# Kernel optimization log

Hardware: AMD Instinct MI355X
Metric: run time of the kernel (lower is better)

Reference implementation:

```python
import jax, jax.numpy as jnp
import numpy as np

N, E, D, H, G, L, EF = 50000, 800000, 128, 256, 512, 3, 8
BN_EPS = 1e-5


def _bn(h, g, b):
    # torch BatchNorm1d in training mode: biased batch stats over the node axis
    m = h.mean(0)
    v = h.var(0)
    return g * (h - m) * jax.lax.rsqrt(v + BN_EPS) + b


def setup_inputs() -> dict:
    ks = jax.random.split(jax.random.key(0), 12)
    sc = 0.05
    return {
        "x": jax.random.normal(ks[0], (N, D), jnp.float32),
        "edge_attr": jax.random.normal(ks[1], (E, EF), jnp.float32),
        "vn_emb": jnp.zeros((1, D), jnp.float32),  # init.constant_(0)
        "We": jax.random.normal(ks[2], (L, EF, D)) * sc,
        "be": jnp.zeros((L, D)),
        "W1": jax.random.normal(ks[3], (L, D, H)) * sc,
        "b1": jnp.zeros((L, H)),
        "g1": jnp.ones((L, H)),
        "bt1": jnp.zeros((L, H)),
        "W2": jax.random.normal(ks[4], (L, H, D)) * sc,
        "b2": jnp.zeros((L, D)),
        "gb": jnp.ones((L, D)),
        "bb": jnp.zeros((L, D)),
        "Wv1": jax.random.normal(ks[5], (L - 1, D, H)) * sc,
        "bv1": jnp.zeros((L - 1, H)),
        "gv1": jnp.ones((L - 1, H)),
        "btv1": jnp.zeros((L - 1, H)),
        "Wv2": jax.random.normal(ks[6], (L - 1, H, D)) * sc,
        "bv2": jnp.zeros((L - 1, D)),
        "gv2": jnp.ones((L - 1, D)),
        "btv2": jnp.zeros((L - 1, D)),
        "edge_index": jax.random.randint(ks[7], (2, E), 0, N),
        "batch": jnp.sort(jax.random.randint(ks[8], (N,), 0, G)),
    }


def reference(x, edge_attr, vn_emb, We, be, W1, b1, g1, bt1, W2, b2, gb, bb,
              Wv1, bv1, gv1, btv1, Wv2, bv2, gv2, btv2, edge_index, batch):
    src, dst = edge_index[0], edge_index[1]
    vn = jnp.broadcast_to(vn_emb, (G, D))  # Embedding(1, D) looked up for every graph
    h = x  # node_encoder is None -> encoded_node = x
    for l in range(L):
        h_in = h + vn[batch]                              # virtual-node broadcast (gather)
        e = edge_attr @ We[l] + be[l]                     # per-layer edge encoder
        msg = jax.nn.relu(h_in[src] + e)                  # GIN message, [E, D]
        aggr = jax.ops.segment_sum(msg, dst, num_segments=N)
        z = h_in + aggr                                   # (1+eps)*h + aggr, eps=0
        z = jax.nn.relu(_bn(z @ W1[l] + b1[l], g1[l], bt1[l]))
        h = _bn(z @ W2[l] + b2[l], gb[l], bb[l])          # conv MLP out + outer BatchNorm
        if l < L - 1:
            h = jax.nn.relu(h)                            # dropout ratio 0 -> identity
            pooled = jax.ops.segment_sum(h_in, batch, num_segments=G) + vn
            t = jax.nn.relu(_bn(pooled @ Wv1[l] + bv1[l], gv1[l], btv1[l]))
            vn = jax.nn.relu(_bn(t @ Wv2[l] + bv2[l], gv2[l], btv2[l]))
    return h  # JK == 'last'
```

## Files before the change

### kernel.cpp

```cpp
#include <hip/hip_runtime.h>
#include <hip/hip_bf16.h>

#define N_NODES 50000
#define N_EDGES 800000
#define DIM 128
#define HID 256
#define N_GRAPH 512
#define N_LAYER 3
#define EFEAT 8
#define BN_EPS 1e-5f
#define MAX_GROUPS 240000
#define AGGR_WAVES 8192

typedef unsigned short u16;
typedef unsigned int u32;

using bf16x8_t = short __attribute__((ext_vector_type(8)));
using f32x4_t  = float __attribute__((ext_vector_type(4)));
using f32x2    = float __attribute__((ext_vector_type(2)));
using f32x4v   = float __attribute__((ext_vector_type(4)));


__device__ __forceinline__ void atomic_add_f(float* p, float v) {
    unsafeAtomicAdd(p, v);
}
__device__ __forceinline__ u16 f2bf(float x) {
    union { float f; u32 u; } v; v.f = x;
    u32 r = v.u + 0x7FFF + ((v.u >> 16) & 1);
    return (u16)(r >> 16);
}
__device__ __forceinline__ float bf2f(u16 u) {
    union { u32 i; float f; } v; v.i = (u32)u << 16; return v.f;
}
__device__ __forceinline__ float2 up2(u32 p) {
    return make_float2(bf2f((u16)(p & 0xFFFF)), bf2f((u16)(p >> 16)));
}
__device__ __forceinline__ u32 pk2(float a, float b) {
    return (u32)f2bf(a) | ((u32)f2bf(b) << 16);
}
__device__ __forceinline__ f32x2 up2p(u32 p) {
    union { u32 u[2]; f32x2 f; } v;
    v.u[0] = p << 16;
    v.u[1] = p & 0xFFFF0000u;
    return v.f;
}
__device__ __forceinline__ f32x2 splat2(float x) {
    f32x2 r; r.x = x; r.y = x; return r;
}

__global__ __launch_bounds__(256) void wconv_kernel(
    const float* __restrict__ W1, const float* __restrict__ W2,
    u16* __restrict__ W1t, u16* __restrict__ W2t)
{
    int idx = blockIdx.x * 256 + threadIdx.x;
    if (idx >= 6 * 32768) return;
    int m = idx >> 15;
    int off = idx & 32767;
    int l = m >> 1;
    if ((m & 1) == 0) {
        int r = off >> 8, c = off & 255;
        W1t[(size_t)l * 32768 + c * 128 + r] = f2bf(W1[(size_t)l * 32768 + r * 256 + c]);
    } else {
        int r = off >> 7, c = off & 127;
        W2t[(size_t)l * 32768 + c * 256 + r] = f2bf(W2[(size_t)l * 32768 + r * 128 + c]);
    }
}

__global__ __launch_bounds__(256) void hist_rank_kernel(
    const int* __restrict__ ei, int* __restrict__ deg, int* __restrict__ rank)
{
    int e = blockIdx.x * 256 + threadIdx.x;
    if (e >= N_EDGES) return;
    int dst = ei[N_EDGES + e];
    rank[e] = atomicAdd(&deg[dst], 1);
}

__global__ __launch_bounds__(1024) void scan_kernel(const int* __restrict__ deg, int* __restrict__ grpptr) {
    __shared__ int wsum[16];
    __shared__ int carry;
    int tid = threadIdx.x;
    if (tid == 0) { carry = 0; grpptr[0] = 0; }
    __syncthreads();
    for (int base = 0; base < N_NODES; base += 1024) {
        int i = base + tid;
        int v = (i < N_NODES) ? ((deg[i] + 3) >> 2) : 0;
        int lane = tid & 63, w = tid >> 6;
        int s = v;
        #pragma unroll
        for (int d = 1; d < 64; d <<= 1) { int t = __shfl_up(s, d); if (lane >= d) s += t; }
        if (lane == 63) wsum[w] = s;
        __syncthreads();
        if (tid < 64) {
            int t = (tid < 16) ? wsum[tid] : 0;
            #pragma unroll
            for (int d = 1; d < 16; d <<= 1) { int u = __shfl_up(t, d); if (tid >= d) t += u; }
            if (tid < 16) wsum[tid] = t;
        }
        __syncthreads();
        int excl = (w > 0) ? wsum[w - 1] : 0;
        int incl = s + excl + carry;
        if (i < N_NODES) grpptr[i + 1] = incl;
        __syncthreads();
        if (tid == 0) carry += wsum[15];
        __syncthreads();
    }
}

__global__ __launch_bounds__(256) void padinit_kernel(uint4* __restrict__ rec4, int nq) {
    int i = blockIdx.x * 256 + threadIdx.x;
    if (i >= nq) return;
    u32 s = (u32)N_NODES << 8;
    rec4[i] = make_uint4(s, 0u, s, 0u);
}

__global__ void negrow_kernel(u16* __restrict__ hin) {
    int l = threadIdx.x;
    *(u32*)(hin + (size_t)N_NODES * DIM + l * 2) = 0xFF7FFF7Fu;
}

__global__ __launch_bounds__(256) void scatter_kernel(
    const int* __restrict__ ei,
    const int* __restrict__ rank, const int* __restrict__ grpptr,
    uint2* __restrict__ srec)
{
    int e = blockIdx.x * 256 + threadIdx.x;
    if (e >= N_EDGES) return;
    int src = __builtin_nontemporal_load(ei + e);
    int dst = __builtin_nontemporal_load(ei + N_EDGES + e);
    int rk  = __builtin_nontemporal_load(rank + e);
    int slot = grpptr[dst] * 4 + rk;
    slot = (grpptr[dst] + (rk >> 2)) * 4 + (rk & 3);
    uint2 v;
    v.x = (u32)src << 8;
    v.y = (u32)e << 5;
    srec[slot] = v;
}

__global__ __launch_bounds__(256) void expand_kernel(
    const uint2* __restrict__ srec, const float* __restrict__ ea,
    char* __restrict__ brec, int nslots)
{
    int i = blockIdx.x * 256 + threadIdx.x;
    if (i >= nslots) return;
    int g = i >> 2;
    int j = i & 3;
    uint2 v = srec[i];
    const char* eaB = (const char*)ea;
    f32x4v lo = *(const f32x4v*)(eaB + v.y);
    f32x4v hi = *(const f32x4v*)(eaB + v.y + 16);
    char* rb = brec + (size_t)g * 144;
    *(u32*)(rb + j * 4) = v.x;
    *(f32x4v*)(rb + 16 + j * 32) = lo;
    *(f32x4v*)(rb + 32 + j * 32) = hi;
}

__global__ __launch_bounds__(256) void wstart_kernel(
    const int* __restrict__ grpptr, int* __restrict__ wstart)
{
    int w = blockIdx.x * 256 + threadIdx.x;
    if (w > AGGR_WAVES) return;
    if (w == AGGR_WAVES) { wstart[w] = N_NODES; return; }
    int Gt = grpptr[N_NODES];
    int q = (int)(((long long)w * Gt) / AGGR_WAVES);
    int lo = 0, hi = N_NODES;
    while (lo < hi) { int mid = (lo + hi) >> 1; if (grpptr[mid] < q) lo = mid + 1; else hi = mid; }
    wstart[w] = lo;
}

template <bool USEBN, int VNM>
__global__ __launch_bounds__(256) void hin_kernel(
    const float* __restrict__ src,
    const float* __restrict__ sum2, const float* __restrict__ ss2,
    const float* __restrict__ g, const float* __restrict__ b, float invN,
    const int* __restrict__ batch,
    const float* __restrict__ vn_emb,
    const float* __restrict__ vnpre, const float* __restrict__ vsum, const float* __restrict__ vss,
    const float* __restrict__ gv, const float* __restrict__ btv, float invG,
    u16* __restrict__ hin, int total4)
{
    int idx = blockIdx.x * 256 + threadIdx.x;
    if (idx >= total4) return;
    int base = idx * 4;
    int n = base >> 7;
    int c = base & (DIM - 1);
    float4 v = *(const float4*)(src + base);
    float o[4] = {v.x, v.y, v.z, v.w};
    if (USEBN) {
        #pragma unroll
        for (int j = 0; j < 4; ++j) {
            int cj = c + j;
            float m = sum2[cj] * invN;
            float var = ss2[cj] * invN - m * m;
            float r = rsqrtf(var + BN_EPS);
            float a = g[cj] * r;
            o[j] = fmaxf(fmaf(a, o[j], b[cj] - m * a), 0.f);
        }
    }
    int grp = batch[n];
    if (VNM == 0) {
        const float4 w = *(const float4*)(vn_emb + c);
        o[0] += w.x; o[1] += w.y; o[2] += w.z; o[3] += w.w;
    } else {
        const float4 vp = *(const float4*)(vnpre + (size_t)grp * DIM + c);
        float vv[4] = {vp.x, vp.y, vp.z, vp.w};
        #pragma unroll
        for (int j = 0; j < 4; ++j) {
            int cj = c + j;
            float m = vsum[cj] * invG;
            float var = vss[cj] * invG - m * m;
            float r = rsqrtf(var + BN_EPS);
            float a = gv[cj] * r;
            o[j] += fmaxf(fmaf(a, vv[j], btv[cj] - m * a), 0.f);
        }
    }
    uint2 pk;
    pk.x = pk2(o[0], o[1]);
    pk.y = pk2(o[2], o[3]);
    *(uint2*)(hin + base) = pk;
}

__device__ __forceinline__ void edge_term_f(
    u32 h, f32x4v ea, f32x4v eb, const f32x2* rW, f32x2 rB, f32x2& acc)
{
    f32x2 ex = rB;
    ex = __builtin_elementwise_fma(splat2(ea.x), rW[0], ex);
    ex = __builtin_elementwise_fma(splat2(ea.y), rW[1], ex);
    ex = __builtin_elementwise_fma(splat2(ea.z), rW[2], ex);
    ex = __builtin_elementwise_fma(splat2(ea.w), rW[3], ex);
    ex = __builtin_elementwise_fma(splat2(eb.x), rW[4], ex);
    ex = __builtin_elementwise_fma(splat2(eb.y), rW[5], ex);
    ex = __builtin_elementwise_fma(splat2(eb.z), rW[6], ex);
    ex = __builtin_elementwise_fma(splat2(eb.w), rW[7], ex);
    f32x2 s = up2p(h) + ex;
    s = __builtin_elementwise_max(s, splat2(0.f));
    acc += s;
}

__global__ __launch_bounds__(256) void aggr_kernel(
    const int* __restrict__ grpptr, const char* __restrict__ rec,
    const float* __restrict__ Wel, const float* __restrict__ bel,
    const u16* __restrict__ hin, u16* __restrict__ z,
    const int* __restrict__ wstart)
{
    const int lane = threadIdx.x & 63;
    const int cb = lane * 4;
    const int wid = __builtin_amdgcn_readfirstlane((blockIdx.x << 2) + (threadIdx.x >> 6));

    f32x2 rW[EFEAT];
    #pragma unroll
    for (int k = 0; k < EFEAT; ++k) {
        float2 t = *(const float2*)(Wel + k * DIM + lane * 2);
        rW[k].x = t.x; rW[k].y = t.y;
    }
    float2 tb = *(const float2*)(bel + lane * 2);
    f32x2 rB; rB.x = tb.x; rB.y = tb.y;

    const char* hinB = (const char*)hin;
    int n = wstart[wid];
    const int n1 = wstart[wid + 1];

    while (n < n1 && grpptr[n + 1] == grpptr[n]) {
        f32x2 a0 = up2p(*(const u32*)(hinB + ((u32)n << 8) + cb));
        *(u32*)(z + ((size_t)n << 7) + lane * 2) = pk2(a0.x, a0.y);
        ++n;
    }
    if (n < n1) {
        int g = grpptr[n];
        const int gTot = grpptr[n1];
        int gEnd = grpptr[n + 1];
        f32x2 acc = up2p(*(const u32*)(hinB + ((u32)n << 8) + cb));
        const char* rb = rec + (size_t)g * 144;

        uint4 so = *(const uint4*)rb;
        u32 h0 = *(const u32*)(hinB + so.x + cb);
        u32 h1 = *(const u32*)(hinB + so.y + cb);
        u32 h2 = *(const u32*)(hinB + so.z + cb);
        u32 h3 = *(const u32*)(hinB + so.w + cb);
        f32x4v e0a = *(const f32x4v*)(rb + 16);
        f32x4v e0b = *(const f32x4v*)(rb + 32);
        f32x4v e1a = *(const f32x4v*)(rb + 48);
        f32x4v e1b = *(const f32x4v*)(rb + 64);
        f32x4v e2a = *(const f32x4v*)(rb + 80);
        f32x4v e2b = *(const f32x4v*)(rb + 96);
        f32x4v e3a = *(const f32x4v*)(rb + 112);
        f32x4v e3b = *(const f32x4v*)(rb + 128);
        uint4 soN = *(const uint4*)(rb + 144);

        #pragma unroll 2
        for (; g < gTot; ++g, rb += 144) {
            u32 i0 = *(const u32*)(hinB + soN.x + cb);
            u32 i1 = *(const u32*)(hinB + soN.y + cb);
            u32 i2 = *(const u32*)(hinB + soN.z + cb);
            u32 i3 = *(const u32*)(hinB + soN.w + cb);
            f32x4v f0a = *(const f32x4v*)(rb + 160);
            f32x4v f0b = *(const f32x4v*)(rb + 176);
            f32x4v f1a = *(const f32x4v*)(rb + 192);
            f32x4v f1b = *(const f32x4v*)(rb + 208);
            f32x4v f2a = *(const f32x4v*)(rb + 224);
            f32x4v f2b = *(const f32x4v*)(rb + 240);
            f32x4v f3a = *(const f32x4v*)(rb + 256);
            f32x4v f3b = *(const f32x4v*)(rb + 272);
            uint4 soNN = *(const uint4*)(rb + 288);
            edge_term_f(h0, e0a, e0b, rW, rB, acc);
            edge_term_f(h1, e1a, e1b, rW, rB, acc);
            edge_term_f(h2, e2a, e2b, rW, rB, acc);
            edge_term_f(h3, e3a, e3b, rW, rB, acc);
            h0 = i0; h1 = i1; h2 = i2; h3 = i3;
            e0a = f0a; e0b = f0b; e1a = f1a; e1b = f1b;
            e2a = f2a; e2b = f2b; e3a = f3a; e3b = f3b;
            soN = soNN;
            if (g + 1 == gEnd) {
                *(u32*)(z + ((size_t)n << 7) + lane * 2) = pk2(acc.x, acc.y);
                ++n;
                if (g + 1 < gTot) {
                    while (grpptr[n + 1] == grpptr[n]) {
                        f32x2 a0 = up2p(*(const u32*)(hinB + ((u32)n << 8) + cb));
                        *(u32*)(z + ((size_t)n << 7) + lane * 2) = pk2(a0.x, a0.y);
                        ++n;
                    }
                    acc = up2p(*(const u32*)(hinB + ((u32)n << 8) + cb));
                    gEnd = grpptr[n + 1];
                }
            }
        }
    }
    while (n < n1) {
        f32x2 a0 = up2p(*(const u32*)(hinB + ((u32)n << 8) + cb));
        *(u32*)(z + ((size_t)n << 7) + lane * 2) = pk2(a0.x, a0.y);
        ++n;
    }
}

template <int MODE, bool CBF16>
__global__ __launch_bounds__(256) void gemm_bf16_kernel(
    const u16* __restrict__ Aa,
    const float* __restrict__ sSum, const float* __restrict__ sSS,
    const float* __restrict__ gA, const float* __restrict__ btA, float invCnt,
    const u16* __restrict__ Bt,
    const float* __restrict__ bias,
    void* __restrict__ CoutV,
    float* __restrict__ outSum, float* __restrict__ outSS,
    int M, int K, int Nc)
{
    constexpr int BM = 128, BN = 128, BK = 128;
    constexpr int LDA = BK + 8;
    __shared__ u16 As[BM * LDA];
    __shared__ u16 Bs[64 * LDA];
    __shared__ float csum[BN], css[BN];

    const int tid = threadIdx.x;
    const int wave = tid >> 6, lane = tid & 63;
    const int row0 = blockIdx.x * BM, col0 = blockIdx.y * BN;
    const int w_m = (wave & 1) * 64, w_n = (wave >> 1) * 32;
    const int quad = lane >> 4, l16 = lane & 15;

    if (tid < BN) { csum[tid] = 0.f; css[tid] = 0.f; }

    f32x4_t acc[4][4];
    #pragma unroll
    for (int mi = 0; mi < 4; ++mi)
        #pragma unroll
        for (int ni = 0; ni < 4; ++ni)
            acc[mi][ni] = (f32x4_t){0.f, 0.f, 0.f, 0.f};

    const int kc = (tid & 15) * 8;
    const int nkt = K / BK;

    for (int kt = 0; kt < nkt; ++kt) {
        float af[8], bf_[8];
        if (MODE == 1) {
            #pragma unroll
            for (int j = 0; j < 8; ++j) {
                int kg = kt * BK + kc + j;
                float m = sSum[kg] * invCnt;
                float var = sSS[kg] * invCnt - m * m;
                float r = rsqrtf(var + BN_EPS);
                float a = gA[kg] * r;
                af[j] = a;
                bf_[j] = btA[kg] - m * a;
            }
        }
        #pragma unroll
        for (int it = 0; it < 8; ++it) {
            int chunk = it * 256 + tid;
            int row = chunk >> 4;
            int gr = row0 + row; if (gr >= M) gr = M - 1;
            uint4 q = *(const uint4*)(Aa + (size_t)gr * K + kt * BK + kc);
            if (MODE == 1) {
                float2 p0 = up2(q.x), p1 = up2(q.y), p2 = up2(q.z), p3 = up2(q.w);
                p0.x = fmaxf(fmaf(af[0], p0.x, bf_[0]), 0.f);
                p0.y = fmaxf(fmaf(af[1], p0.y, bf_[1]), 0.f);
                p1.x = fmaxf(fmaf(af[2], p1.x, bf_[2]), 0.f);
                p1.y = fmaxf(fmaf(af[3], p1.y, bf_[3]), 0.f);
                p2.x = fmaxf(fmaf(af[4], p2.x, bf_[4]), 0.f);
                p2.y = fmaxf(fmaf(af[5], p2.y, bf_[5]), 0.f);
                p3.x = fmaxf(fmaf(af[6], p3.x, bf_[6]), 0.f);
                p3.y = fmaxf(fmaf(af[7], p3.y, bf_[7]), 0.f);
                q.x = pk2(p0.x, p0.y); q.y = pk2(p1.x, p1.y);
                q.z = pk2(p2.x, p2.y); q.w = pk2(p3.x, p3.y);
            }
            *(uint4*)(As + row * LDA + kc) = q;
        }
        #pragma unroll
        for (int half = 0; half < 2; ++half) {
            #pragma unroll
            for (int it = 0; it < 4; ++it) {
                int chunk = it * 256 + tid;
                int n = chunk >> 4;
                uint4 q = *(const uint4*)(Bt + (size_t)(col0 + half * 64 + n) * K + kt * BK + kc);
                *(uint4*)(Bs + n * LDA + kc) = q;
            }
            __syncthreads();
            #pragma unroll
            for (int ks = 0; ks < 4; ++ks) {
                bf16x8_t a_frag[4], b_frag[2];
                #pragma unroll
                for (int mi = 0; mi < 4; ++mi)
                    a_frag[mi] = *(const bf16x8_t*)(As + (w_m + mi * 16 + l16) * LDA + ks * 32 + quad * 8);
                #pragma unroll
                for (int ni = 0; ni < 2; ++ni)
                    b_frag[ni] = *(const bf16x8_t*)(Bs + (w_n + ni * 16 + l16) * LDA + ks * 32 + quad * 8);
                #pragma unroll
                for (int mi = 0; mi < 4; ++mi)
                    #pragma unroll
                    for (int ni = 0; ni < 2; ++ni)
                        acc[mi][half * 2 + ni] = __builtin_amdgcn_mfma_f32_16x16x32_bf16(
                            a_frag[mi], b_frag[ni], acc[mi][half * 2 + ni], 0, 0, 0);
            }
            __syncthreads();
        }
    }

    u16* Cb = (u16*)CoutV;
    float* Cf = (float*)CoutV;
    #pragma unroll
    for (int half = 0; half < 2; ++half)
    #pragma unroll
    for (int ni = 0; ni < 2; ++ni) {
        int ccol = half * 64 + w_n + ni * 16 + l16;
        int col = col0 + ccol;
        float bv = bias[col];
        float s = 0.f, qs = 0.f;
        #pragma unroll
        for (int mi = 0; mi < 4; ++mi) {
            int rbase = row0 + w_m + mi * 16 + quad * 4;
            #pragma unroll
            for (int reg = 0; reg < 4; ++reg) {
                int gr = rbase + reg;
                if (gr < M) {
                    float o = acc[mi][half * 2 + ni][reg] + bv;
                    s += o;
                    qs += o * o;
                    if (CBF16) Cb[(size_t)gr * Nc + col] = f2bf(o);
                    else       Cf[(size_t)gr * Nc + col] = o;
                }
            }
        }
        s += __shfl_xor(s, 16);  s += __shfl_xor(s, 32);
        qs += __shfl_xor(qs, 16);  qs += __shfl_xor(qs, 32);
        if (quad == 0) {
            atomicAdd(&csum[ccol], s);
            atomicAdd(&css[ccol], qs);
        }
    }
    __syncthreads();
    if (tid < BN) {
        atomic_add_f(outSum + col0 + tid, csum[tid]);
        atomic_add_f(outSS + col0 + tid, css[tid]);
    }
}

template <int MODE>
__global__ __launch_bounds__(256) void gemm_kernel(
    const float* __restrict__ Aa,
    const float* __restrict__ sSum, const float* __restrict__ sSS,
    const float* __restrict__ gA, const float* __restrict__ btA, float invCnt,
    const float* __restrict__ B, const float* __restrict__ bias,
    float* __restrict__ Cout, float* __restrict__ outSum, float* __restrict__ outSS,
    int M, int K, int Nc)
{
    __shared__ float As[16][68];
    __shared__ float Bs[16][64];
    __shared__ float alphaS[256], betaS[256];
    __shared__ float csum[64], css[64];

    const int tid = threadIdx.x;
    const int tx = tid & 15, ty = tid >> 4;
    const int row0 = blockIdx.x * 64, col0 = blockIdx.y * 64;

    if (tid < 64) { csum[tid] = 0.f; css[tid] = 0.f; }
    if (MODE == 1) {
        for (int k = tid; k < K; k += 256) {
            float m = sSum[k] * invCnt;
            float var = sSS[k] * invCnt - m * m;
            float r = rsqrtf(var + BN_EPS);
            float a = gA[k] * r;
            alphaS[k] = a;
            betaS[k] = btA[k] - m * a;
        }
    }
    __syncthreads();

    float acc[4][4];
    #pragma unroll
    for (int i = 0; i < 4; ++i)
        #pragma unroll
        for (int j = 0; j < 4; ++j) acc[i][j] = 0.f;

    const int lr = tid >> 2;
    const int lk = (tid & 3) * 4;
    const int bk = tid >> 4;
    const int bc = tx * 4;

    for (int kt = 0; kt < K; kt += 16) {
        int gr = row0 + lr;
        float4 va = make_float4(0.f, 0.f, 0.f, 0.f);
        if (gr < M) {
            va = *(const float4*)(Aa + (size_t)gr * K + kt + lk);
            if (MODE == 1) {
                int k0 = kt + lk;
                va.x = fmaxf(fmaf(alphaS[k0 + 0], va.x, betaS[k0 + 0]), 0.f);
                va.y = fmaxf(fmaf(alphaS[k0 + 1], va.y, betaS[k0 + 1]), 0.f);
                va.z = fmaxf(fmaf(alphaS[k0 + 2], va.z, betaS[k0 + 2]), 0.f);
                va.w = fmaxf(fmaf(alphaS[k0 + 3], va.w, betaS[k0 + 3]), 0.f);
            }
        }
        As[lk + 0][lr] = va.x;
        As[lk + 1][lr] = va.y;
        As[lk + 2][lr] = va.z;
        As[lk + 3][lr] = va.w;
        const float4 vb4 = *(const float4*)(B + (size_t)(kt + bk) * Nc + col0 + bc);
        *(float4*)&Bs[bk][bc] = vb4;
        __syncthreads();
        #pragma unroll
        for (int kk = 0; kk < 16; ++kk) {
            const float4 a4 = *(const float4*)&As[kk][ty * 4];
            const float4 b4 = *(const float4*)&Bs[kk][tx * 4];
            float av[4] = {a4.x, a4.y, a4.z, a4.w};
            float bv4[4] = {b4.x, b4.y, b4.z, b4.w};
            #pragma unroll
            for (int i = 0; i < 4; ++i)
                #pragma unroll
                for (int j = 0; j < 4; ++j)
                    acc[i][j] = fmaf(av[i], bv4[j], acc[i][j]);
        }
        __syncthreads();
    }

    const float4 bvv = *(const float4*)(bias + col0 + tx * 4);
    float bias4[4] = {bvv.x, bvv.y, bvv.z, bvv.w};
    float ps[4] = {0.f, 0.f, 0.f, 0.f};
    float pq[4] = {0.f, 0.f, 0.f, 0.f};
    #pragma unroll
    for (int i = 0; i < 4; ++i) {
        int gr = row0 + ty * 4 + i;
        if (gr < M) {
            float o[4];
            #pragma unroll
            for (int j = 0; j < 4; ++j) {
                o[j] = acc[i][j] + bias4[j];
                ps[j] += o[j];
                pq[j] += o[j] * o[j];
            }
            *(float4*)(Cout + (size_t)gr * Nc + col0 + tx * 4) = make_float4(o[0], o[1], o[2], o[3]);
        }
    }
    #pragma unroll
    for (int j = 0; j < 4; ++j) {
        atomicAdd(&csum[tx * 4 + j], ps[j]);
        atomicAdd(&css[tx * 4 + j], pq[j]);
    }
    __syncthreads();
    if (tid < 64) {
        atomic_add_f(outSum + col0 + tid, csum[tid]);
        atomic_add_f(outSS + col0 + tid, css[tid]);
    }
}

template <int VNM>
__global__ __launch_bounds__(64) void pooled_seg_kernel(
    const u16* __restrict__ hin, const int* __restrict__ batch,
    const float* __restrict__ vn_emb,
    const float* __restrict__ vnpre, const float* __restrict__ vsum, const float* __restrict__ vss,
    const float* __restrict__ gv, const float* __restrict__ btv, float invG,
    float* __restrict__ pooled)
{
    int g = blockIdx.x;
    int lane = threadIdx.x;
    int c2 = lane * 2;
    int lo = 0, hi = N_NODES;
    while (lo < hi) { int mid = (lo + hi) >> 1; if (batch[mid] < g) lo = mid + 1; else hi = mid; }
    int start = lo;
    hi = N_NODES;
    while (lo < hi) { int mid = (lo + hi) >> 1; if (batch[mid] < g + 1) lo = mid + 1; else hi = mid; }
    int end = lo;

    f32x2 acc;
    if (VNM == 0) {
        float2 w = *(const float2*)(vn_emb + c2);
        acc.x = w.x; acc.y = w.y;
    } else {
        float2 vs = *(const float2*)(vsum + c2);
        float2 vq = *(const float2*)(vss + c2);
        float2 gg = *(const float2*)(gv + c2);
        float2 bt = *(const float2*)(btv + c2);
        float2 vp = *(const float2*)(vnpre + (size_t)g * DIM + c2);
        float m0 = vs.x * invG, m1 = vs.y * invG;
        float va0 = vq.x * invG - m0 * m0, va1 = vq.y * invG - m1 * m1;
        float a0 = gg.x * rsqrtf(va0 + BN_EPS), a1 = gg.y * rsqrtf(va1 + BN_EPS);
        acc.x = fmaxf(fmaf(a0, vp.x, bt.x - m0 * a0), 0.f);
        acc.y = fmaxf(fmaf(a1, vp.y, bt.y - m1 * a1), 0.f);
    }

    const char* hinB = (const char*)hin;
    const int cb = lane * 4;
    f32x2 s0 = splat2(0.f), s1 = splat2(0.f), s2 = splat2(0.f), s3 = splat2(0.f);
    int n = start;
    for (; n + 3 < end; n += 4) {
        s0 += up2p(*(const u32*)(hinB + ((size_t)(n + 0) << 8) + cb));
        s1 += up2p(*(const u32*)(hinB + ((size_t)(n + 1) << 8) + cb));
        s2 += up2p(*(const u32*)(hinB + ((size_t)(n + 2) << 8) + cb));
        s3 += up2p(*(const u32*)(hinB + ((size_t)(n + 3) << 8) + cb));
    }
    for (; n < end; ++n) s0 += up2p(*(const u32*)(hinB + ((size_t)n << 8) + cb));
    acc += (s0 + s1) + (s2 + s3);
    *(float2*)(pooled + (size_t)g * DIM + c2) = make_float2(acc.x, acc.y);
}

__global__ __launch_bounds__(256) void final_bn_kernel(
    float* __restrict__ outp, const float* __restrict__ sum2, const float* __restrict__ ss2,
    const float* __restrict__ g, const float* __restrict__ b, float invN, int total4)
{
    int idx = blockIdx.x * 256 + threadIdx.x;
    if (idx >= total4) return;
    int base = idx * 4;
    int c = base & (DIM - 1);
    float4 v = *(const float4*)(outp + base);
    float o[4] = {v.x, v.y, v.z, v.w};
    #pragma unroll
    for (int j = 0; j < 4; ++j) {
        int cj = c + j;
        float m = sum2[cj] * invN;
        float var = ss2[cj] * invN - m * m;
        float r = rsqrtf(var + BN_EPS);
        float a = g[cj] * r;
        o[j] = fmaf(a, o[j], b[cj] - m * a);
    }
    *(float4*)(outp + base) = make_float4(o[0], o[1], o[2], o[3]);
}

extern "C" void kernel_launch(void* const* d_in, const int* in_sizes, int n_in,
                              void* d_out, int out_size, void* d_ws, size_t ws_size,
                              hipStream_t stream) {
    const float* x         = (const float*)d_in[0];
    const float* edge_attr = (const float*)d_in[1];
    const float* vn_emb    = (const float*)d_in[2];
    const float* We        = (const float*)d_in[3];
    const float* be        = (const float*)d_in[4];
    const float* W1        = (const float*)d_in[5];
    const float* b1        = (const float*)d_in[6];
    const float* g1v       = (const float*)d_in[7];
    const float* bt1       = (const float*)d_in[8];
    const float* W2        = (const float*)d_in[9];
    const float* b2        = (const float*)d_in[10];
    const float* gb        = (const float*)d_in[11];
    const float* bb        = (const float*)d_in[12];
    const float* Wv1       = (const float*)d_in[13];
    const float* bv1       = (const float*)d_in[14];
    const float* gv1       = (const float*)d_in[15];
    const float* btv1      = (const float*)d_in[16];
    const float* Wv2       = (const float*)d_in[17];
    const float* bv2       = (const float*)d_in[18];
    const float* gv2       = (const float*)d_in[19];
    const float* btv2      = (const float*)d_in[20];
    const int* edge_index  = (const int*)d_in[21];
    const int* batch       = (const int*)d_in[22];
    float* outp = (float*)d_out;

    auto au = [](size_t x) { return (x + 255) & ~(size_t)255; };
    char* p = (char*)d_ws;
    u16* h_in   = (u16*)p;  p += au((size_t)(N_NODES + 1) * DIM * 2);
    u16* z_bf   = (u16*)p;  p += au((size_t)N_NODES * DIM * 2);
    u16* c1_bf  = (u16*)p;  p += au((size_t)N_NODES * HID * 2);
    u16* W1t    = (u16*)p;  p += au((size_t)3 * 32768 * 2);
    u16* W2t    = (u16*)p;  p += au((size_t)3 * 32768 * 2);
    float* pooled = (float*)p;  p += au((size_t)N_GRAPH * DIM * 4);
    float* tpre   = (float*)p;  p += au((size_t)N_GRAPH * HID * 4);
    float* vnpre  = (float*)p;  p += au((size_t)N_GRAPH * DIM * 4);
    float* stats  = (float*)p;  p += au(2048 * 4);
    float* sum1 = stats,        *ss1 = stats + 256;
    float* sum2 = stats + 512,  *ss2 = stats + 640;
    float* vsum1 = stats + 768, *vss1 = stats + 1024;
    float* vsum2 = stats + 1280, *vss2 = stats + 1408;
    int* grpptr = (int*)p;  p += au((size_t)(N_NODES + 1) * 4);
    int* wstart = (int*)p;  p += au((size_t)(AGGR_WAVES + 1) * 4);
    char* brec  = p;        p += au((size_t)(MAX_GROUPS + 4) * 144 + 512);
    int* deg   = (int*)z_bf;
    int* rank  = (int*)c1_bf;
    uint2* srec = (uint2*)(c1_bf + au((size_t)N_EDGES * 4) / 2);

    const float invN = 1.0f / (float)N_NODES;
    const float invG = 1.0f / (float)N_GRAPH;
    const int total4 = N_NODES * DIM / 4;
    const int nslots = (MAX_GROUPS + 4) * 4;

    hipMemsetAsync(deg, 0, N_NODES * sizeof(int), stream);
    hist_rank_kernel<<<(N_EDGES + 255) / 256, 256, 0, stream>>>(edge_index, deg, rank);
    scan_kernel<<<1, 1024, 0, stream>>>(deg, grpptr);
    padinit_kernel<<<(nslots / 2 + 255) / 256, 256, 0, stream>>>((uint4*)srec, nslots / 2);
    negrow_kernel<<<1, 64, 0, stream>>>(h_in);
    scatter_kernel<<<(N_EDGES + 255) / 256, 256, 0, stream>>>(
        edge_index, rank, grpptr, srec);
    expand_kernel<<<(nslots + 255) / 256, 256, 0, stream>>>(
        srec, edge_attr, brec, nslots);
    wstart_kernel<<<(AGGR_WAVES + 256) / 256, 256, 0, stream>>>(grpptr, wstart);
    wconv_kernel<<<768, 256, 0, stream>>>(W1, W2, W1t, W2t);

    const int AGGR_BLOCKS = AGGR_WAVES / 4;

    for (int l = 0; l < N_LAYER; ++l) {
        if (l == 0)
            hin_kernel<false, 0><<<(total4 + 255) / 256, 256, 0, stream>>>(
                x, nullptr, nullptr, nullptr, nullptr, 0.f, batch,
                vn_emb, nullptr, nullptr, nullptr, nullptr, nullptr, 0.f,
                h_in, total4);
        else
            hin_kernel<true, 1><<<(total4 + 255) / 256, 256, 0, stream>>>(
                outp, sum2, ss2, gb + (size_t)(l - 1) * DIM, bb + (size_t)(l - 1) * DIM, invN, batch,
                nullptr, vnpre, vsum2, vss2,
                gv2 + (size_t)(l - 1) * DIM, btv2 + (size_t)(l - 1) * DIM, invG,
                h_in, total4);

        if (l == 0)
            pooled_seg_kernel<0><<<N_GRAPH, 64, 0, stream>>>(
                h_in, batch, vn_emb, nullptr, nullptr, nullptr, nullptr, nullptr, 0.f, pooled);
        else if (l < N_LAYER - 1)
            pooled_seg_kernel<1><<<N_GRAPH, 64, 0, stream>>>(
                h_in, batch, nullptr, vnpre, vsum2, vss2,
                gv2 + (size_t)(l - 1) * DIM, btv2 + (size_t)(l - 1) * DIM, invG, pooled);

        hipMemsetAsync(stats, 0, 2048 * sizeof(float), stream);

        aggr_kernel<<<AGGR_BLOCKS, 256, 0, stream>>>(
            grpptr, brec, We + (size_t)l * EFEAT * DIM, be + (size_t)l * DIM,
            h_in, z_bf, wstart);

        dim3 g1d((N_NODES + 127) / 128, HID / 128);
        gemm_bf16_kernel<0, true><<<g1d, 256, 0, stream>>>(
            z_bf, nullptr, nullptr, nullptr, nullptr, 0.f,
            W1t + (size_t)l * 32768, b1 + (size_t)l * HID,
            (void*)c1_bf, sum1, ss1, N_NODES, DIM, HID);

        dim3 g2d((N_NODES + 127) / 128, DIM / 128);
        gemm_bf16_kernel<1, false><<<g2d, 256, 0, stream>>>(
            c1_bf, sum1, ss1, g1v + (size_t)l * HID, bt1 + (size_t)l * HID, invN,
            W2t + (size_t)l * 32768, b2 + (size_t)l * DIM,
            (void*)outp, sum2, ss2, N_NODES, HID, DIM);

        if (l < N_LAYER - 1) {
            dim3 g3d(N_GRAPH / 64, HID / 64);
            gemm_kernel<0><<<g3d, 256, 0, stream>>>(
                pooled, nullptr, nullptr, nullptr, nullptr, 0.f,
                Wv1 + (size_t)l * DIM * HID, bv1 + (size_t)l * HID,
                tpre, vsum1, vss1, N_GRAPH, DIM, HID);

            dim3 g4d(N_GRAPH / 64, DIM / 64);
            gemm_kernel<1><<<g4d, 256, 0, stream>>>(
                tpre, vsum1, vss1, gv1 + (size_t)l * HID, btv1 + (size_t)l * HID, invG,
                Wv2 + (size_t)l * HID * DIM, bv2 + (size_t)l * DIM,
                vnpre, vsum2, vss2, N_GRAPH, HID, DIM);
        }
    }

    final_bn_kernel<<<(total4 + 255) / 256, 256, 0, stream>>>(
        outp, sum2, ss2, gb + (size_t)2 * DIM, bb + (size_t)2 * DIM, invN, total4);
}
```

Baseline: 779.1 us.

## Parallelize degree scan across blocks and fold small init kernels into neighbors

Replaces the single-block serial scan over all nodes with a three-kernel multi-block scan (block scans, scan of block sums, add offsets). It also merges the negative-row init into padinit and moves the per-layer stats memset into block 0 of aggr_kernel. The goal is to remove a long single-workgroup serial loop and cut launch and memset overhead. Zeroing stats inside aggr relies on the following GEMM kernels running after aggr has finished, which stream ordering provides.

```diff
diff --git a/kernel.cpp b/kernel.cpp
--- a/kernel.cpp
+++ b/kernel.cpp
@@ -11,6 +11,7 @@
 #define BN_EPS 1e-5f
 #define MAX_GROUPS 240000
 #define AGGR_WAVES 8192
+#define SCAN_BLOCKS ((N_NODES + 1023) / 1024)
 
 typedef unsigned short u16;
 typedef unsigned int u32;
@@ -75,47 +76,59 @@
     rank[e] = atomicAdd(&deg[dst], 1);
 }
 
-__global__ __launch_bounds__(1024) void scan_kernel(const int* __restrict__ deg, int* __restrict__ grpptr) {
+__global__ __launch_bounds__(1024) void scan1_kernel(
+    const int* __restrict__ deg, int* __restrict__ grpptr, int* __restrict__ bsum)
+{
     __shared__ int wsum[16];
-    __shared__ int carry;
+    int blk = blockIdx.x, tid = threadIdx.x;
+    int i = blk * 1024 + tid;
+    int v = (i < N_NODES) ? ((deg[i] + 3) >> 2) : 0;
+    int lane = tid & 63, w = tid >> 6;
+    int s = v;
+    #pragma unroll
+    for (int d = 1; d < 64; d <<= 1) { int t = __shfl_up(s, d); if (lane >= d) s += t; }
+    if (lane == 63) wsum[w] = s;
+    __syncthreads();
+    if (tid < 64) {
+        int t = (tid < 16) ? wsum[tid] : 0;
+        #pragma unroll
+        for (int d = 1; d < 16; d <<= 1) { int u = __shfl_up(t, d); if (tid >= d) t += u; }
+        if (tid < 16) wsum[tid] = t;
+    }
+    __syncthreads();
+    int excl = (w > 0) ? wsum[w - 1] : 0;
+    int incl = s + excl;
+    if (i < N_NODES) grpptr[i + 1] = incl;
+    if (tid == 1023) bsum[blk] = incl;
+}
+
+__global__ __launch_bounds__(64) void scan2_kernel(int* __restrict__ bsum) {
     int tid = threadIdx.x;
-    if (tid == 0) { carry = 0; grpptr[0] = 0; }
-    __syncthreads();
-    for (int base = 0; base < N_NODES; base += 1024) {
-        int i = base + tid;
-        int v = (i < N_NODES) ? ((deg[i] + 3) >> 2) : 0;
-        int lane = tid & 63, w = tid >> 6;
-        int s = v;
-        #pragma unroll
-        for (int d = 1; d < 64; d <<= 1) { int t = __shfl_up(s, d); if (lane >= d) s += t; }
-        if (lane == 63) wsum[w] = s;
-        __syncthreads();
-        if (tid < 64) {
-            int t = (tid < 16) ? wsum[tid] : 0;
-            #pragma unroll
-            for (int d = 1; d < 16; d <<= 1) { int u = __shfl_up(t, d); if (tid >= d) t += u; }
-            if (tid < 16) wsum[tid] = t;
-        }
-        __syncthreads();
-        int excl = (w > 0) ? wsum[w - 1] : 0;
-        int incl = s + excl + carry;
-        if (i < N_NODES) grpptr[i + 1] = incl;
-        __syncthreads();
-        if (tid == 0) carry += wsum[15];
-        __syncthreads();
-    }
-}
-
-__global__ __launch_bounds__(256) void padinit_kernel(uint4* __restrict__ rec4, int nq) {
+    int v = (tid < SCAN_BLOCKS) ? bsum[tid] : 0;
+    int s = v;
+    #pragma unroll
+    for (int d = 1; d < 64; d <<= 1) { int t = __shfl_up(s, d); if (tid >= d) s += t; }
+    if (tid < SCAN_BLOCKS) bsum[tid] = s - v;
+}
+
+__global__ __launch_bounds__(1024) void scan3_kernel(
+    int* __restrict__ grpptr, const int* __restrict__ bsum)
+{
+    int blk = blockIdx.x;
+    int i = blk * 1024 + threadIdx.x;
+    if (i < N_NODES) grpptr[i + 1] += bsum[blk];
+    if (blk == 0 && threadIdx.x == 0) grpptr[0] = 0;
+}
+
+__global__ __launch_bounds__(256) void padinit_kernel(
+    uint4* __restrict__ rec4, int nq, u16* __restrict__ hin)
+{
     int i = blockIdx.x * 256 + threadIdx.x;
+    if (blockIdx.x == 0 && threadIdx.x < 64)
+        *(u32*)(hin + (size_t)N_NODES * DIM + threadIdx.x * 2) = 0xFF7FFF7Fu;
     if (i >= nq) return;
     u32 s = (u32)N_NODES << 8;
     rec4[i] = make_uint4(s, 0u, s, 0u);
-}
-
-__global__ void negrow_kernel(u16* __restrict__ hin) {
-    int l = threadIdx.x;
-    *(u32*)(hin + (size_t)N_NODES * DIM + l * 2) = 0xFF7FFF7Fu;
 }
 
 __global__ __launch_bounds__(256) void scatter_kernel(
@@ -128,8 +141,7 @@
     int src = __builtin_nontemporal_load(ei + e);
     int dst = __builtin_nontemporal_load(ei + N_EDGES + e);
     int rk  = __builtin_nontemporal_load(rank + e);
-    int slot = grpptr[dst] * 4 + rk;
-    slot = (grpptr[dst] + (rk >> 2)) * 4 + (rk & 3);
+    int slot = (grpptr[dst] + (rk >> 2)) * 4 + (rk & 3);
     uint2 v;
     v.x = (u32)src << 8;
     v.y = (u32)e << 5;
@@ -240,11 +252,16 @@
     const int* __restrict__ grpptr, const char* __restrict__ rec,
     const float* __restrict__ Wel, const float* __restrict__ bel,
     const u16* __restrict__ hin, u16* __restrict__ z,
-    const int* __restrict__ wstart)
+    const int* __restrict__ wstart, float* __restrict__ stats)
 {
     const int lane = threadIdx.x & 63;
     const int cb = lane * 4;
     const int wid = __builtin_amdgcn_readfirstlane((blockIdx.x << 2) + (threadIdx.x >> 6));
+
+    if (blockIdx.x == 0) {
+        #pragma unroll
+        for (int i = 0; i < 8; ++i) stats[i * 256 + threadIdx.x] = 0.f;
+    }
 
     f32x2 rW[EFEAT];
     #pragma unroll
@@ -694,6 +711,7 @@
     float* vsum2 = stats + 1280, *vss2 = stats + 1408;
     int* grpptr = (int*)p;  p += au((size_t)(N_NODES + 1) * 4);
     int* wstart = (int*)p;  p += au((size_t)(AGGR_WAVES + 1) * 4);
+    int* bsum   = (int*)p;  p += au((size_t)SCAN_BLOCKS * 4);
     char* brec  = p;        p += au((size_t)(MAX_GROUPS + 4) * 144 + 512);
     int* deg   = (int*)z_bf;
     int* rank  = (int*)c1_bf;
@@ -706,9 +724,10 @@
 
     hipMemsetAsync(deg, 0, N_NODES * sizeof(int), stream);
     hist_rank_kernel<<<(N_EDGES + 255) / 256, 256, 0, stream>>>(edge_index, deg, rank);
-    scan_kernel<<<1, 1024, 0, stream>>>(deg, grpptr);
-    padinit_kernel<<<(nslots / 2 + 255) / 256, 256, 0, stream>>>((uint4*)srec, nslots / 2);
-    negrow_kernel<<<1, 64, 0, stream>>>(h_in);
+    scan1_kernel<<<SCAN_BLOCKS, 1024, 0, stream>>>(deg, grpptr, bsum);
+    scan2_kernel<<<1, 64, 0, stream>>>(bsum);
+    scan3_kernel<<<SCAN_BLOCKS, 1024, 0, stream>>>(grpptr, bsum);
+    padinit_kernel<<<(nslots / 2 + 255) / 256, 256, 0, stream>>>((uint4*)srec, nslots / 2, h_in);
     scatter_kernel<<<(N_EDGES + 255) / 256, 256, 0, stream>>>(
         edge_index, rank, grpptr, srec);
     expand_kernel<<<(nslots + 255) / 256, 256, 0, stream>>>(
@@ -739,11 +758,9 @@
                 h_in, batch, nullptr, vnpre, vsum2, vss2,
                 gv2 + (size_t)(l - 1) * DIM, btv2 + (size_t)(l - 1) * DIM, invG, pooled);
 
-        hipMemsetAsync(stats, 0, 2048 * sizeof(float), stream);
-
         aggr_kernel<<<AGGR_BLOCKS, 256, 0, stream>>>(
             grpptr, brec, We + (size_t)l * EFEAT * DIM, be + (size_t)l * DIM,
-            h_in, z_bf, wstart);
+            h_in, z_bf, wstart, stats);
 
         dim3 g1d((N_NODES + 127) / 128, HID / 128);
         gemm_bf16_kernel<0, true><<<g1d, 256, 0, stream>>>(
```

Result: faster. 732.2 us (-6.0%).
